# Performance work log

Hardware: AMD Instinct MI355X
Metric: run time of the kernel (lower is better)

Reference implementation:

```python
import jax, jax.numpy as jnp
import numpy as np
import math

CH = 256
HEADS = 4
GROUPS = 8
EPS = 1e-5


def group_norm(x, gamma, beta):
    # x: [B, C, H, W], normalize over (C//G, H, W) per group
    B, C, H, W = x.shape
    xg = x.reshape(B, GROUPS, C // GROUPS, H, W)
    mean = xg.mean(axis=(2, 3, 4), keepdims=True)
    var = xg.var(axis=(2, 3, 4), keepdims=True)
    xn = ((xg - mean) * jax.lax.rsqrt(var + EPS)).reshape(B, C, H, W)
    return xn * gamma[None, :, None, None] + beta[None, :, None, None]


def setup_inputs() -> dict:
    key = jax.random.key(0)
    ks = jax.random.split(key, 7)
    B, C, H, W = 4, CH, 64, 64
    x = jax.random.normal(ks[0], (B, C, H, W), dtype=jnp.float32)
    norm_w = jnp.ones((C,), dtype=jnp.float32)
    norm_b = jnp.zeros((C,), dtype=jnp.float32)
    s = 1.0 / math.sqrt(C)
    qkv_w = jax.random.normal(ks[1], (3 * C, C), dtype=jnp.float32) * s  # 1x1 conv kernel
    qkv_b = jnp.zeros((3 * C,), dtype=jnp.float32)
    proj_w = jax.random.normal(ks[2], (C, C), dtype=jnp.float32) * s
    proj_b = jnp.zeros((C,), dtype=jnp.float32)
    return {"x": x, "norm_w": norm_w, "norm_b": norm_b,
            "qkv_w": qkv_w, "qkv_b": qkv_b,
            "proj_w": proj_w, "proj_b": proj_b}


def reference(x, norm_w, norm_b, qkv_w, qkv_b, proj_w, proj_b):
    B, C, H, W = x.shape
    d = C // HEADS
    h = group_norm(x, norm_w, norm_b)
    # 1x1 conv == channel matmul
    qkv = jnp.einsum('oc,bchw->bohw', qkv_w, h) + qkv_b[None, :, None, None]
    qkv = qkv.reshape(B, 3, HEADS, d, H * W)
    q, k, v = qkv[:, 0], qkv[:, 1], qkv[:, 2]  # [B, heads, d, HW]
    attn = jnp.einsum('bhdi,bhdj->bhij', q, k) / jnp.sqrt(jnp.float32(d))
    attn = jax.nn.softmax(attn, axis=-1)
    out = jnp.einsum('bhij,bhdj->bhdi', attn, v).reshape(B, C, H, W)
    out = jnp.einsum('oc,bchw->bohw', proj_w, out) + proj_b[None, :, None, None]
    return x + out
```

## Files before the change

### kernel.cpp

```cpp
#include <hip/hip_runtime.h>
#include <stdint.h>

#define NB    4
#define CC    256
#define NN    4096
#define NHEAD 4
#define DH    64
#define NGRP  8
#define GSIZE 131072

typedef unsigned short u16;
typedef __attribute__((ext_vector_type(8))) short s16x8;
typedef __attribute__((ext_vector_type(4))) float f32x4;

__device__ __forceinline__ u16 f2b(float f) {
  uint32_t x = __float_as_uint(f);
  x += 0x7fffu + ((x >> 16) & 1u);
  return (u16)(x >> 16);
}

__device__ __forceinline__ uint32_t pk2(float a, float b) {
  uint32_t r;
  asm("v_cvt_pk_bf16_f32 %0, %1, %2" : "=v"(r) : "v"(a), "v"(b));
  return r;
}

__global__ __launch_bounds__(256) void k_prep(const float* __restrict__ qw,
                                              const float* __restrict__ pw,
                                              u16* __restrict__ qwb,
                                              u16* __restrict__ pwb,
                                              float* __restrict__ stats) {
  int i = blockIdx.x * 256 + threadIdx.x;
  if (i < 64) stats[i] = 0.f;
  for (int idx = i; idx < 3 * CC * CC; idx += 65536) qwb[idx] = f2b(qw[idx]);
  if (i < CC * CC) pwb[i] = f2b(pw[i]);
}

__global__ __launch_bounds__(256) void k_gn_stats(const float* __restrict__ x,
                                                  float* __restrict__ stats) {
  int grp = blockIdx.x >> 4, sub = blockIdx.x & 15;
  const float4* p4 = (const float4*)(x + (size_t)grp * GSIZE + (size_t)sub * 8192);
  float s = 0.f, s2 = 0.f;
#pragma unroll
  for (int i = 0; i < 8; ++i) {
    float4 v = p4[threadIdx.x + 256 * i];
    s  += v.x + v.y + v.z + v.w;
    s2 += v.x * v.x + v.y * v.y + v.z * v.z + v.w * v.w;
  }
#pragma unroll
  for (int off = 1; off < 64; off <<= 1) { s += __shfl_xor(s, off); s2 += __shfl_xor(s2, off); }
  __shared__ float red[8];
  int w = threadIdx.x >> 6;
  if ((threadIdx.x & 63) == 0) { red[w] = s; red[4 + w] = s2; }
  __syncthreads();
  if (threadIdx.x == 0) {
    s  = red[0] + red[1] + red[2] + red[3];
    s2 = red[4] + red[5] + red[6] + red[7];
    atomicAdd(&stats[grp], s);
    atomicAdd(&stats[32 + grp], s2);
  }
}

__global__ __launch_bounds__(256) void k_gn_norm(const float* __restrict__ x,
                                                 const float* __restrict__ stats,
                                                 const float* __restrict__ gw,
                                                 const float* __restrict__ gb,
                                                 u16* __restrict__ ht) {
  __shared__ u16 T[64 * 72];
  int b = blockIdx.z, cb = blockIdx.y, nb = blockIdx.x;
  int t = threadIdx.x;
  int c = t >> 2, nch = (t & 3) * 16;
  int cg = cb * 64 + c;
  int grp = b * NGRP + (cg >> 5);
  float mean = stats[grp] * (1.f / (float)GSIZE);
  float var  = stats[32 + grp] * (1.f / (float)GSIZE) - mean * mean;
  float rstd = rsqrtf(var + 1e-5f);
  float ga = gw[cg] * rstd;
  float be = gb[cg] - mean * ga;
  const float* px = x + ((size_t)b * CC + cg) * NN + nb * 64 + nch;
#pragma unroll
  for (int k = 0; k < 4; ++k) {
    float4 v = *(const float4*)(px + 4 * k);
    int nl = nch + 4 * k;
    T[(nl + 0) * 72 + c] = f2b(v.x * ga + be);
    T[(nl + 1) * 72 + c] = f2b(v.y * ga + be);
    T[(nl + 2) * 72 + c] = f2b(v.z * ga + be);
    T[(nl + 3) * 72 + c] = f2b(v.w * ga + be);
  }
  __syncthreads();
  int n = t >> 2, cch = (t & 3) * 16;
  u16* dst = ht + ((size_t)b * NN + nb * 64 + n) * CC + cb * 64 + cch;
  *(uint4*)(dst)     = *(const uint4*)&T[n * 72 + cch];
  *(uint4*)(dst + 8) = *(const uint4*)&T[n * 72 + cch + 8];
}

__global__ __launch_bounds__(256) void k_qkv(const u16* __restrict__ Aw,
                                             const float* __restrict__ bias,
                                             const u16* __restrict__ ht,
                                             u16* __restrict__ Qt,
                                             u16* __restrict__ Kt,
                                             u16* __restrict__ Vv) {
  __shared__ u16 sm[5120];
  u16* As = sm;
  u16* Bs = sm + 2560;
  int b = blockIdx.z, bm = blockIdx.y, bn = blockIdx.x;
  int t = threadIdx.x, w = t >> 6, lane = t & 63, lr = lane & 15, lg = lane >> 4;
  int wm = w >> 1, wn = w & 1;
  int srow = t >> 2, sch = (t & 3) * 8;
  const u16* Ap = Aw + (size_t)(bm * 64 + srow) * CC + sch;
  const u16* Bp = ht + ((size_t)b * NN + bn * 64 + srow) * CC + sch;
  f32x4 acc[2][2] = {};
  for (int kt = 0; kt < CC / 32; ++kt) {
    *(uint4*)&As[srow * 40 + sch] = *(const uint4*)(Ap + kt * 32);
    *(uint4*)&Bs[srow * 40 + sch] = *(const uint4*)(Bp + kt * 32);
    __syncthreads();
    s16x8 af[2], bf[2];
#pragma unroll
    for (int fm = 0; fm < 2; ++fm) af[fm] = *(const s16x8*)&As[(wm * 32 + fm * 16 + lr) * 40 + lg * 8];
#pragma unroll
    for (int fn = 0; fn < 2; ++fn) bf[fn] = *(const s16x8*)&Bs[(wn * 32 + fn * 16 + lr) * 40 + lg * 8];
#pragma unroll
    for (int fm = 0; fm < 2; ++fm)
#pragma unroll
      for (int fn = 0; fn < 2; ++fn)
        acc[fm][fn] = __builtin_amdgcn_mfma_f32_16x16x32_bf16(af[fm], bf[fn], acc[fm][fn], 0, 0, 0);
    __syncthreads();
  }
  int which = bm >> 2, head = bm & 3;
  if (which == 2) {
#pragma unroll
    for (int fm = 0; fm < 2; ++fm)
#pragma unroll
      for (int fn = 0; fn < 2; ++fn)
#pragma unroll
        for (int r = 0; r < 4; ++r) {
          int m = wm * 32 + fm * 16 + lg * 4 + r;
          int n = wn * 32 + fn * 16 + lr;
          float v = acc[fm][fn][r] + bias[bm * 64 + m];
          Vv[((size_t)(b * NHEAD + head) * DH + m) * NN + bn * 64 + n] = f2b(v);
        }
  } else {
    u16* Ts = sm;
    float scale = (which == 0) ? 0.125f * 1.44269504f : 1.0f;
#pragma unroll
    for (int fm = 0; fm < 2; ++fm)
#pragma unroll
      for (int fn = 0; fn < 2; ++fn)
#pragma unroll
        for (int r = 0; r < 4; ++r) {
          int m = wm * 32 + fm * 16 + lg * 4 + r;
          int n = wn * 32 + fn * 16 + lr;
          float v = (acc[fm][fn][r] + bias[bm * 64 + m]) * scale;
          Ts[n * 72 + m] = f2b(v);
        }
    __syncthreads();
    u16* dst = (which == 0 ? Qt : Kt);
    int n = t >> 2, cch = (t & 3) * 16;
    u16* o = dst + ((size_t)(b * NHEAD + head) * NN + bn * 64 + n) * DH + cch;
    *(uint4*)(o)     = *(const uint4*)&Ts[n * 72 + cch];
    *(uint4*)(o + 8) = *(const uint4*)&Ts[n * 72 + cch + 8];
  }
}

__global__ __launch_bounds__(512, 4) void k_attn(const u16* __restrict__ Qt,
                                                 const u16* __restrict__ Kt,
                                                 const u16* __restrict__ Vv,
                                                 u16* __restrict__ att) {
  __shared__ __align__(16) u16 sm[18432];
  int bh = blockIdx.y, qt = blockIdx.x;
  int t = threadIdx.x, w = t >> 6, lane = t & 63, lr = lane & 15, lg = lane >> 4;
  int wq = w & 3, h = w >> 2;
  const u16* Qb = Qt + ((size_t)bh * NN + qt * 128 + wq * 32) * DH;
  const u16* Kb = Kt + (size_t)bh * NN * DH;
  const u16* Vb = Vv + (size_t)bh * DH * NN;
  s16x8 bq0[2], bq1[2];
#pragma unroll
  for (int kk = 0; kk < 2; ++kk) {
    bq0[kk] = *(const s16x8*)(Qb + lr * DH + kk * 32 + lg * 8);
    bq1[kk] = *(const s16x8*)(Qb + (16 + lr) * DH + kk * 32 + lg * 8);
  }
  const s16x8 ones = (s16x8)(short)0x3F80;
  f32x4 oacc[2][4] = {};
  f32x4 la0 = {}, la1 = {};
  u16* Ksh = sm + h * 9216;
  u16* Vsh = sm + h * 9216 + 4608;
  int tl = t & 255;
  int srow = tl >> 2, sch = (tl & 3) * 16;
  int prow = (srow & 32) | (((srow >> 2) & 3) << 3) | (((srow >> 4) & 1) << 2) | (srow & 3);
  int jbase = h * 2048;
  const u16* kp0 = Kb + (size_t)(jbase + prow) * DH + sch;
  const u16* vp0 = Vb + (size_t)srow * NN + jbase + sch;
  u16* ksw = Ksh + srow * 72 + sch;
  u16* vsw = Vsh + srow * 72 + sch;
  {
    uint4 a0 = *(const uint4*)(kp0), a1 = *(const uint4*)(kp0 + 8);
    uint4 b0 = *(const uint4*)(vp0), b1 = *(const uint4*)(vp0 + 8);
    *(uint4*)(ksw) = a0; *(uint4*)(ksw + 8) = a1;
    *(uint4*)(vsw) = b0; *(uint4*)(vsw + 8) = b1;
  }
  __syncthreads();
  for (int j0 = 0; j0 < 2048; j0 += 64) {
    int jn = (j0 + 64 < 2048) ? j0 + 64 : 0;
    const u16* kp = kp0 + (size_t)jn * DH;
    const u16* vp = vp0 + jn;
    uint4 rka = *(const uint4*)(kp), rkb = *(const uint4*)(kp + 8);
    uint4 rva = *(const uint4*)(vp), rvb = *(const uint4*)(vp + 8);
    f32x4 s0[4], s1[4];
    __builtin_amdgcn_s_setprio(1);
#pragma unroll
    for (int q = 0; q < 4; ++q) {
      const u16* base = Ksh + (q * 16 + lr) * 72 + lg * 8;
      s16x8 a0 = *(const s16x8*)(base);
      s16x8 a1 = *(const s16x8*)(base + 32);
      f32x4 z0 = {}, z1 = {};
      z0 = __builtin_amdgcn_mfma_f32_16x16x32_bf16(a0, bq0[0], z0, 0, 0, 0);
      z1 = __builtin_amdgcn_mfma_f32_16x16x32_bf16(a0, bq1[0], z1, 0, 0, 0);
      z0 = __builtin_amdgcn_mfma_f32_16x16x32_bf16(a1, bq0[1], z0, 0, 0, 0);
      z1 = __builtin_amdgcn_mfma_f32_16x16x32_bf16(a1, bq1[1], z1, 0, 0, 0);
      s0[q] = z0; s1[q] = z1;
    }
    __builtin_amdgcn_s_setprio(0);
    union { s16x8 v; uint32_t u[4]; } pb0[2], pb1[2];
#pragma unroll
    for (int q = 0; q < 4; ++q) {
      float a0 = exp2f(s0[q][0]);
      float a1 = exp2f(s0[q][1]);
      float a2 = exp2f(s0[q][2]);
      float a3 = exp2f(s0[q][3]);
      float b0 = exp2f(s1[q][0]);
      float b1 = exp2f(s1[q][1]);
      float b2 = exp2f(s1[q][2]);
      float b3 = exp2f(s1[q][3]);
      int c = (q >> 1) & 1;
      pb0[c].u[(q & 1) * 2]     = pk2(a0, a1);
      pb0[c].u[(q & 1) * 2 + 1] = pk2(a2, a3);
      pb1[c].u[(q & 1) * 2]     = pk2(b0, b1);
      pb1[c].u[(q & 1) * 2 + 1] = pk2(b2, b3);
    }
    __builtin_amdgcn_s_setprio(1);
#pragma unroll
    for (int dt = 0; dt < 4; ++dt) {
      const u16* vb2 = Vsh + (dt * 16 + lr) * 72 + lg * 8;
#pragma unroll
      for (int c = 0; c < 2; ++c) {
        s16x8 av = *(const s16x8*)(vb2 + c * 32);
        oacc[0][dt] = __builtin_amdgcn_mfma_f32_16x16x32_bf16(av, pb0[c].v, oacc[0][dt], 0, 0, 0);
        oacc[1][dt] = __builtin_amdgcn_mfma_f32_16x16x32_bf16(av, pb1[c].v, oacc[1][dt], 0, 0, 0);
      }
    }
#pragma unroll
    for (int c = 0; c < 2; ++c) {
      la0 = __builtin_amdgcn_mfma_f32_16x16x32_bf16(ones, pb0[c].v, la0, 0, 0, 0);
      la1 = __builtin_amdgcn_mfma_f32_16x16x32_bf16(ones, pb1[c].v, la1, 0, 0, 0);
    }
    __builtin_amdgcn_s_setprio(0);
    __syncthreads();
    *(uint4*)(ksw) = rka; *(uint4*)(ksw + 8) = rkb;
    *(uint4*)(vsw) = rva; *(uint4*)(vsw + 8) = rvb;
    __syncthreads();
  }
  float* F = (float*)sm;
  float* slot = F + (wq * 64 + lane) * 36;
  if (h == 1) {
#pragma unroll
    for (int g = 0; g < 2; ++g)
#pragma unroll
      for (int dt = 0; dt < 4; ++dt)
#pragma unroll
        for (int r = 0; r < 4; ++r) slot[g * 16 + dt * 4 + r] = oacc[g][dt][r];
    slot[32] = la0[0];
    slot[33] = la1[0];
  }
  __syncthreads();
  if (h == 0) {
    int b = bh >> 2, hd = bh & 3;
#pragma unroll
    for (int g = 0; g < 2; ++g) {
      float lA = g ? la1[0] : la0[0];
      float lB = slot[32 + g];
      float linv = 1.f / (lA + lB);
      u16* ob = att + ((size_t)b * NN + qt * 128 + wq * 32 + g * 16 + lr) * CC + hd * 64 + lg * 4;
#pragma unroll
      for (int dt = 0; dt < 4; ++dt) {
        float o0 = (oacc[g][dt][0] + slot[g * 16 + dt * 4 + 0]) * linv;
        float o1 = (oacc[g][dt][1] + slot[g * 16 + dt * 4 + 1]) * linv;
        float o2 = (oacc[g][dt][2] + slot[g * 16 + dt * 4 + 2]) * linv;
        float o3 = (oacc[g][dt][3] + slot[g * 16 + dt * 4 + 3]) * linv;
        uint2 pkd;
        pkd.x = pk2(o0, o1);
        pkd.y = pk2(o2, o3);
        *(uint2*)(ob + dt * 16) = pkd;
      }
    }
  }
}

__global__ __launch_bounds__(256) void k_proj(const u16* __restrict__ Aw,
                                              const float* __restrict__ bias,
                                              const u16* __restrict__ att,
                                              const float* __restrict__ x,
                                              float* __restrict__ out) {
  __shared__ u16 sm[5120];
  u16* As = sm;
  u16* Bs = sm + 2560;
  int b = blockIdx.z, bm = blockIdx.y, bn = blockIdx.x;
  int t = threadIdx.x, w = t >> 6, lane = t & 63, lr = lane & 15, lg = lane >> 4;
  int wm = w >> 1, wn = w & 1;
  int srow = t >> 2, sch = (t & 3) * 8;
  const u16* Ap = Aw + (size_t)(bm * 64 + srow) * CC + sch;
  const u16* Bp = att + ((size_t)b * NN + bn * 64 + srow) * CC + sch;
  f32x4 acc[2][2] = {};
  for (int kt = 0; kt < CC / 32; ++kt) {
    *(uint4*)&As[srow * 40 + sch] = *(const uint4*)(Ap + kt * 32);
    *(uint4*)&Bs[srow * 40 + sch] = *(const uint4*)(Bp + kt * 32);
    __syncthreads();
    s16x8 af[2], bf[2];
#pragma unroll
    for (int fm = 0; fm < 2; ++fm) af[fm] = *(const s16x8*)&As[(wm * 32 + fm * 16 + lr) * 40 + lg * 8];
#pragma unroll
    for (int fn = 0; fn < 2; ++fn) bf[fn] = *(const s16x8*)&Bs[(wn * 32 + fn * 16 + lr) * 40 + lg * 8];
#pragma unroll
    for (int fm = 0; fm < 2; ++fm)
#pragma unroll
      for (int fn = 0; fn < 2; ++fn)
        acc[fm][fn] = __builtin_amdgcn_mfma_f32_16x16x32_bf16(af[fm], bf[fn], acc[fm][fn], 0, 0, 0);
    __syncthreads();
  }
#pragma unroll
  for (int fm = 0; fm < 2; ++fm)
#pragma unroll
    for (int fn = 0; fn < 2; ++fn)
#pragma unroll
      for (int r = 0; r < 4; ++r) {
        int o = bm * 64 + wm * 32 + fm * 16 + lg * 4 + r;
        int n = bn * 64 + wn * 32 + fn * 16 + lr;
        size_t idx = ((size_t)b * CC + o) * NN + n;
        out[idx] = x[idx] + bias[o] + acc[fm][fn][r];
      }
}

extern "C" void kernel_launch(void* const* d_in, const int* in_sizes, int n_in,
                              void* d_out, int out_size, void* d_ws, size_t ws_size,
                              hipStream_t stream) {
  const float* x  = (const float*)d_in[0];
  const float* nw = (const float*)d_in[1];
  const float* nb = (const float*)d_in[2];
  const float* qw = (const float*)d_in[3];
  const float* qb = (const float*)d_in[4];
  const float* pw = (const float*)d_in[5];
  const float* pb = (const float*)d_in[6];
  float* out = (float*)d_out;
  char* ws = (char*)d_ws;
  float* stats = (float*)(ws + 0);
  u16* qwb = (u16*)(ws + 4096);
  u16* pwb = (u16*)(ws + 397312);
  u16* ht  = (u16*)(ws + 528384);
  u16* Qt  = (u16*)(ws + 8916992);
  u16* Kt  = (u16*)(ws + 17305600);
  u16* Vv  = (u16*)(ws + 25694208);
  u16* att = (u16*)(ws + 34082816);

  k_prep<<<dim3(256), dim3(256), 0, stream>>>(qw, pw, qwb, pwb, stats);
  k_gn_stats<<<dim3(512), dim3(256), 0, stream>>>(x, stats);
  k_gn_norm<<<dim3(64, 4, NB), dim3(256), 0, stream>>>(x, stats, nw, nb, ht);
  k_qkv<<<dim3(64, 12, NB), dim3(256), 0, stream>>>(qwb, qb, ht, Qt, Kt, Vv);
  k_attn<<<dim3(32, NB * NHEAD), dim3(512), 0, stream>>>(Qt, Kt, Vv, att);
  k_proj<<<dim3(64, 4, NB), dim3(256), 0, stream>>>(pwb, pb, att, x, out);
}
```

Baseline: 147.9 us.

## Split attention KV range across two blocks and merge partials in new kernel

The attention kernel now splits each query tile's key range across two blocks (grid z=2), with each block handling 1024 keys split between its two wave halves. Unnormalised partial outputs (bf16) and row sums go to a scratch buffer, the output buffer reused as Opart, and a new merge kernel sums them, normalises and writes the att layout. This doubles the grid from 512 to 1024 blocks to fill more of the GPU's CUs. In exchange it adds an extra kernel launch, extra global traffic, and an extra bf16 rounding of the partials before normalisation. The merge adds partials without rescaling, which is only correct if the two halves share a common max reference, as the original two-wave merge already assumed.

```diff
diff --git a/kernel.cpp b/kernel.cpp
--- a/kernel.cpp
+++ b/kernel.cpp
@@ -165,9 +165,10 @@
 __global__ __launch_bounds__(512, 4) void k_attn(const u16* __restrict__ Qt,
                                                  const u16* __restrict__ Kt,
                                                  const u16* __restrict__ Vv,
-                                                 u16* __restrict__ att) {
+                                                 u16* __restrict__ Opart,
+                                                 float* __restrict__ lpart) {
   __shared__ __align__(16) u16 sm[18432];
-  int bh = blockIdx.y, qt = blockIdx.x;
+  int bh = blockIdx.y, qt = blockIdx.x, sK = blockIdx.z;
   int t = threadIdx.x, w = t >> 6, lane = t & 63, lr = lane & 15, lg = lane >> 4;
   int wq = w & 3, h = w >> 2;
   const u16* Qb = Qt + ((size_t)bh * NN + qt * 128 + wq * 32) * DH;
@@ -187,7 +188,7 @@
   int tl = t & 255;
   int srow = tl >> 2, sch = (tl & 3) * 16;
   int prow = (srow & 32) | (((srow >> 2) & 3) << 3) | (((srow >> 4) & 1) << 2) | (srow & 3);
-  int jbase = h * 2048;
+  int jbase = sK * 2048 + h * 1024;
   const u16* kp0 = Kb + (size_t)(jbase + prow) * DH + sch;
   const u16* vp0 = Vb + (size_t)srow * NN + jbase + sch;
   u16* ksw = Ksh + srow * 72 + sch;
@@ -199,8 +200,8 @@
     *(uint4*)(vsw) = b0; *(uint4*)(vsw + 8) = b1;
   }
   __syncthreads();
-  for (int j0 = 0; j0 < 2048; j0 += 64) {
-    int jn = (j0 + 64 < 2048) ? j0 + 64 : 0;
+  for (int j0 = 0; j0 < 1024; j0 += 64) {
+    int jn = (j0 + 64 < 1024) ? j0 + 64 : 0;
     const u16* kp = kp0 + (size_t)jn * DH;
     const u16* vp = vp0 + jn;
     uint4 rka = *(const uint4*)(kp), rkb = *(const uint4*)(kp + 8);
@@ -273,19 +274,20 @@
   }
   __syncthreads();
   if (h == 0) {
-    int b = bh >> 2, hd = bh & 3;
+    int blk = (qt * 16 + bh) * 2 + sK;
 #pragma unroll
     for (int g = 0; g < 2; ++g) {
       float lA = g ? la1[0] : la0[0];
       float lB = slot[32 + g];
-      float linv = 1.f / (lA + lB);
-      u16* ob = att + ((size_t)b * NN + qt * 128 + wq * 32 + g * 16 + lr) * CC + hd * 64 + lg * 4;
+      int row = blk * 128 + wq * 32 + g * 16 + lr;
+      if (lg == 0) lpart[row] = lA + lB;
+      u16* ob = Opart + (size_t)row * 64 + lg * 4;
 #pragma unroll
       for (int dt = 0; dt < 4; ++dt) {
-        float o0 = (oacc[g][dt][0] + slot[g * 16 + dt * 4 + 0]) * linv;
-        float o1 = (oacc[g][dt][1] + slot[g * 16 + dt * 4 + 1]) * linv;
-        float o2 = (oacc[g][dt][2] + slot[g * 16 + dt * 4 + 2]) * linv;
-        float o3 = (oacc[g][dt][3] + slot[g * 16 + dt * 4 + 3]) * linv;
+        float o0 = oacc[g][dt][0] + slot[g * 16 + dt * 4 + 0];
+        float o1 = oacc[g][dt][1] + slot[g * 16 + dt * 4 + 1];
+        float o2 = oacc[g][dt][2] + slot[g * 16 + dt * 4 + 2];
+        float o3 = oacc[g][dt][3] + slot[g * 16 + dt * 4 + 3];
         uint2 pkd;
         pkd.x = pk2(o0, o1);
         pkd.y = pk2(o2, o3);
@@ -293,6 +295,34 @@
       }
     }
   }
+}
+
+__global__ __launch_bounds__(256) void k_mrg(const u16* __restrict__ Opart,
+                                             const float* __restrict__ lpart,
+                                             u16* __restrict__ att) {
+  int gid = blockIdx.x * 256 + threadIdx.x;
+  int row = gid >> 3, ch = gid & 7;
+  int qrow = row & 127, qtbh = row >> 7;
+  int qt = qtbh >> 4, bh = qtbh & 15;
+  int b = bh >> 2, hd = bh & 3;
+  int rA = qtbh * 256 + qrow, rB = rA + 128;
+  float linv = 1.f / (lpart[rA] + lpart[rB]);
+  uint4 pa = *(const uint4*)(Opart + (size_t)rA * 64 + ch * 8);
+  uint4 pb = *(const uint4*)(Opart + (size_t)rB * 64 + ch * 8);
+  uint32_t ua[4] = {pa.x, pa.y, pa.z, pa.w};
+  uint32_t ub[4] = {pb.x, pb.y, pb.z, pb.w};
+  uint4 o;
+  uint32_t* po = (uint32_t*)&o;
+#pragma unroll
+  for (int i = 0; i < 4; ++i) {
+    float a0 = __uint_as_float(ua[i] << 16);
+    float a1 = __uint_as_float(ua[i] & 0xffff0000u);
+    float b0 = __uint_as_float(ub[i] << 16);
+    float b1 = __uint_as_float(ub[i] & 0xffff0000u);
+    po[i] = pk2((a0 + b0) * linv, (a1 + b1) * linv);
+  }
+  u16* dst = att + ((size_t)b * NN + qt * 128 + qrow) * CC + hd * 64 + ch * 8;
+  *(uint4*)dst = o;
 }
 
 __global__ __launch_bounds__(256) void k_proj(const u16* __restrict__ Aw,
@@ -359,11 +389,14 @@
   u16* Kt  = (u16*)(ws + 17305600);
   u16* Vv  = (u16*)(ws + 25694208);
   u16* att = (u16*)(ws + 34082816);
+  float* lpart = (float*)(ws + 42471424);
+  u16* Opart = (u16*)d_out;
 
   k_prep<<<dim3(256), dim3(256), 0, stream>>>(qw, pw, qwb, pwb, stats);
   k_gn_stats<<<dim3(512), dim3(256), 0, stream>>>(x, stats);
   k_gn_norm<<<dim3(64, 4, NB), dim3(256), 0, stream>>>(x, stats, nw, nb, ht);
   k_qkv<<<dim3(64, 12, NB), dim3(256), 0, stream>>>(qwb, qb, ht, Qt, Kt, Vv);
-  k_attn<<<dim3(32, NB * NHEAD), dim3(512), 0, stream>>>(Qt, Kt, Vv, att);
+  k_attn<<<dim3(32, NB * NHEAD, 2), dim3(512), 0, stream>>>(Qt, Kt, Vv, Opart, lpart);
+  k_mrg<<<dim3(2048), dim3(256), 0, stream>>>(Opart, lpart, att);
   k_proj<<<dim3(64, 4, NB), dim3(256), 0, stream>>>(pwb, pb, att, x, out);
 }
```

Result: slower. 154.8 us (+4.7%).
